# Optimization experiments

Measured on AMD Instinct MI355X. Metric: run time of the kernel, lower is better.

The kernel has to match this reference:

```python
import jax, jax.numpy as jnp
import numpy as np

TEMPERATURE = 0.1
MAX_POS = 6
MAX_NEG = 30
POS_NEG_RATIO = 1.0
NEG_K = max(6, MAX_NEG)  # static top-k width for negatives


def setup_inputs() -> dict:
    key = jax.random.key(0)
    k1, k2 = jax.random.split(key)
    K, D = 8192, 256
    features = jax.random.normal(k1, (K, D), dtype=jnp.float32)
    labels = jax.random.randint(k2, (K,), 0, 64, dtype=jnp.int64)
    return {"features": features, "labels": labels}


def reference(features, labels):
    K = features.shape[0]
    # L2-normalize embeddings (F.normalize, dim=1)
    f = features / jnp.clip(jnp.linalg.norm(features, axis=1, keepdims=True), 1e-12)
    sim = jnp.matmul(f, f.T) / TEMPERATURE                      # [K, K]
    sim = sim - jax.lax.stop_gradient(jnp.max(sim, axis=1, keepdims=True))
    exp_sim = jnp.exp(sim)

    eye = jnp.eye(K, dtype=bool)
    same = labels[:, None] == labels[None, :]
    mask_pos = same & ~eye                                      # same label, off-diagonal
    mask_neg = ~same                                            # 1 - mask_pos - eye

    n_pos = jnp.sum(mask_pos, axis=1).astype(jnp.int32)         # [K]
    n_neg = jnp.sum(mask_neg, axis=1).astype(jnp.int32)         # [K]

    # per-anchor dynamic sample counts (vectorized version of the python loop)
    max_pos_i = jnp.minimum(
        n_pos,
        jnp.maximum(1, jnp.minimum(MAX_POS, (n_neg.astype(jnp.float32) * POS_NEG_RATIO).astype(jnp.int32))),
    )
    max_neg_i = jnp.minimum(n_neg, NEG_K)
    valid_row = (n_pos > 0) & (n_neg > 0)
    max_pos_i = jnp.where(valid_row, max_pos_i, 0)
    max_neg_i = jnp.where(valid_row, max_neg_i, 0)

    rows = jnp.arange(K)[:, None]
    neg_inf = jnp.finfo(sim.dtype).min

    # top-k hard positives by similarity, masked to the first max_pos_i ranks
    pos_scores = jnp.where(mask_pos, sim, neg_inf)
    _, pos_idx = jax.lax.top_k(pos_scores, MAX_POS)             # [K, MAX_POS]
    pos_keep = (jnp.arange(MAX_POS)[None, :] < max_pos_i[:, None]).astype(sim.dtype)
    new_mask_pos = jnp.zeros((K, K), sim.dtype).at[rows, pos_idx].add(pos_keep)

    # random negatives: randperm emulated by top-k of uniform scores over neg slots
    rand = jax.random.uniform(jax.random.key(42), (K, K), dtype=jnp.float32)
    neg_scores = jnp.where(mask_neg, rand, -1.0)
    _, neg_idx = jax.lax.top_k(neg_scores, NEG_K)               # [K, NEG_K]
    neg_keep = (jnp.arange(NEG_K)[None, :] < max_neg_i[:, None]).astype(sim.dtype)
    new_mask_neg = jnp.zeros((K, K), sim.dtype).at[rows, neg_idx].add(neg_keep)

    numerator = jnp.sum(exp_sim * new_mask_pos, axis=1)
    denominator = jnp.sum(exp_sim * (new_mask_pos + new_mask_neg), axis=1)
    loss = -jnp.log(jnp.clip(numerator / denominator, 1e-8))
    return jnp.mean(loss)
```

## Files before the change

kernel.cpp:

```cpp
#include <hip/hip_runtime.h>
#include <hip/hip_fp16.h>
#include <math.h>
#include <stdint.h>


#define NEGK 30
#define MAXP 6
#define MAXBC 320
#define GT 64

typedef _Float16 h2v __attribute__((ext_vector_type(2)));
typedef _Float16 f16x8 __attribute__((ext_vector_type(8)));
typedef float f32x16 __attribute__((ext_vector_type(16)));

__device__ __forceinline__ uint64_t mix64(uint64_t z) {
  z += 0x9E3779B97F4A7C15ULL;
  z = (z ^ (z >> 30)) * 0xBF58476D1CE4E5B9ULL;
  z = (z ^ (z >> 27)) * 0x94D049BB133111EBULL;
  return z ^ (z >> 31);
}

__device__ __forceinline__ float wave_reduce_add(float p) {
#pragma unroll
  for (int o = 32; o; o >>= 1) p += __shfl_down(p, o, 64);
  return p;
}

__device__ __forceinline__ float dot8h(uint4 a, uint4 b, float acc) {
  const h2v* pa = (const h2v*)&a;
  const h2v* pb = (const h2v*)&b;
#if __has_builtin(__builtin_amdgcn_fdot2)
#pragma unroll
  for (int q = 0; q < 4; ++q) acc = __builtin_amdgcn_fdot2(pa[q], pb[q], acc, false);
#else
#pragma unroll
  for (int q = 0; q < 4; ++q)
    acc += (float)pa[q].x * (float)pb[q].x + (float)pa[q].y * (float)pb[q].y;
#endif
  return acc;
}

__global__ __launch_bounds__(256) void k_prep(const float* __restrict__ F,
                                              const int* __restrict__ labels, int K,
                                              __half* __restrict__ Fh,
                                              int* __restrict__ g_start,
                                              int* __restrict__ g_soff,
                                              int* __restrict__ g_bucket,
                                              int4* __restrict__ g_meta) {
  __shared__ int cnt[64], start[65], cur[64], soff_s[64];
  const int tid = threadIdx.x;

  if ((int)blockIdx.x < K / 4) {
    const int row = blockIdx.x * 4 + (tid >> 6);
    const int lane = tid & 63;
    const float4 a = ((const float4*)(F + (size_t)row * 256))[lane];
    float p = a.x * a.x + a.y * a.y + a.z * a.z + a.w * a.w;
    p = wave_reduce_add(p);
    p = __shfl(p, 0, 64);
    const float inv = 1.0f / fmaxf(sqrtf(p), 1e-12f);
    union { __half2 h[2]; uint2 u; } cv;
    cv.h[0] = __float22half2_rn(make_float2(a.x * inv, a.y * inv));
    cv.h[1] = __float22half2_rn(make_float2(a.z * inv, a.w * inv));
    ((uint2*)(Fh + (size_t)row * 256))[lane] = cv.u;
    return;
  }

  if (tid < 64) cnt[tid] = 0;
  __syncthreads();
  for (int t = tid; t < K; t += 256) atomicAdd(&cnt[labels[t] & 63], 1);
  __syncthreads();
  if (tid == 0) {
    int acc = 0, sacc = 0;
    for (int l = 0; l < 64; ++l) {
      start[l] = acc;
      const int B = cnt[l];
      acc += B;
      soff_s[l] = sacc;
      const int Bc = B < MAXBC ? B : MAXBC;
      sacc += Bc * Bc;
    }
    start[64] = acc;
  }
  __syncthreads();
  if (tid < 64) { cur[tid] = start[tid]; g_soff[tid] = soff_s[tid]; }
  if (tid < 65) g_start[tid] = start[tid];
  __syncthreads();
  for (int t = tid; t < K; t += 256) {
    const int l = labels[t] & 63;
    const int p = atomicAdd(&cur[l], 1);
    g_bucket[p] = t;
    g_meta[t] = make_int4(start[l], cnt[l], p - start[l], soff_s[l]);
  }
}

__global__ __launch_bounds__(256, 4) void k_gram(const __half* __restrict__ Fh,
                                                 const int* __restrict__ g_start,
                                                 const int* __restrict__ g_soff,
                                                 const int* __restrict__ g_bucket,
                                                 float* __restrict__ g_sims) {
  const int b  = blockIdx.x;
  const int bs = g_start[b];
  const int B  = g_start[b + 1] - bs;
  const int Bc = B < MAXBC ? B : MAXBC;
  if (Bc <= 0) return;
  const int r0 = blockIdx.y * GT;
  const int c0 = blockIdx.z * GT;
  if (r0 >= Bc || c0 >= Bc) return;

  const int tid = threadIdx.x;
  const int wv = tid >> 6, lane = tid & 63;
  const int wr = (wv >> 1) * 32;
  const int wc = (wv & 1) * 32;
  const int rA = r0 + wr + (lane & 31);
  const int rB = c0 + wc + (lane & 31);
  const int kq = lane >> 5;

  const int gA = g_bucket[bs + (rA < Bc ? rA : Bc - 1)];
  const int gB = g_bucket[bs + (rB < Bc ? rB : Bc - 1)];
  const uint4* pA = (const uint4*)(Fh + (size_t)gA * 256) + kq;
  const uint4* pB = (const uint4*)(Fh + (size_t)gB * 256) + kq;

  f32x16 acc;
#pragma unroll
  for (int q = 0; q < 16; ++q) acc[q] = 0.0f;

#pragma unroll
  for (int it = 0; it < 16; ++it) {
    const f16x8 a  = *(const f16x8*)(pA + 2 * it);
    const f16x8 bf = *(const f16x8*)(pB + 2 * it);
    acc = __builtin_amdgcn_mfma_f32_32x32x16_f16(a, bf, acc, 0, 0, 0);
  }

  float* outb = g_sims + g_soff[b];
  const int ccs = c0 + wc + (lane & 31);
  const bool cok = ccs < Bc;
#pragma unroll
  for (int reg = 0; reg < 16; ++reg) {
    const int row = (reg & 3) + 8 * (reg >> 2) + 4 * (lane >> 5);
    const int rrs = r0 + wr + row;
    if (cok && rrs < Bc)
      outb[(size_t)rrs * Bc + ccs] = (rrs == ccs) ? -3.0e38f : acc[reg] * 10.0f;
  }
}

__global__ __launch_bounds__(256) void k_anchor(
    const __half* __restrict__ Fh, const int* __restrict__ g_bucket,
    const int4* __restrict__ g_meta, const float* __restrict__ g_sims,
    float* __restrict__ g_part, int K) {
  __shared__ uint4 sA[4 * 32];
  const int wv = threadIdx.x >> 6;
  const int lane = threadIdx.x & 63;
  const int i = blockIdx.x * 4 + wv;

  ((uint2*)sA)[wv * 64 + lane] = ((const uint2*)(Fh + (size_t)i * 256))[lane];
  const uint4* sw = sA + wv * 32;

  const int4 mt = g_meta[i];
  const int bs = mt.x, B = mt.y;
  const int Bc = B < MAXBC ? B : MAXBC;
  int loc = mt.z;
  if (loc >= Bc) loc = 0;
  const int n_pos = B - 1;
  const int n_neg = K - B;
  const float* simrow = g_sims + mt.w + (size_t)loc * Bc;

  float v[5];
#pragma unroll
  for (int rr = 0; rr < 5; ++rr) {
    const int t = lane + rr * 64;
    v[rr] = (t < Bc) ? simrow[t] : -3.4e38f;
  }

  int t6 = n_neg < MAXP ? n_neg : MAXP;
  if (t6 < 1) t6 = 1;
  int take = n_pos < t6 ? n_pos : t6;
  if (n_pos <= 0 || n_neg <= 0) take = 0;
  const int target = (take > 0) ? (n_neg < NEGK ? n_neg : NEGK) : 0;

  const int s = lane & 3, g = lane >> 2;
  const int n0 = g, n1 = 16 + g;
  const uint64_t z0 = mix64(((uint64_t)(uint32_t)i << 32) | (uint32_t)n0);
  const uint64_t z1 = mix64(((uint64_t)(uint32_t)i << 32) | (uint32_t)n1);
  const unsigned int r0 = (unsigned int)(((uint64_t)(uint32_t)z0 * (uint64_t)n_neg) >> 32);
  const unsigned int r1 = (unsigned int)(((uint64_t)(uint32_t)z1 * (uint64_t)n_neg) >> 32);
  const int pos0 = (r0 < (unsigned int)bs) ? (int)r0 : (int)r0 + B;
  const int pos1 = (r1 < (unsigned int)bs) ? (int)r1 : (int)r1 + B;
  const bool pv0 = (n0 < target), pv1 = (n1 < target);
  const int j0 = pv0 ? g_bucket[pos0] : 0;
  const int j1 = pv1 ? g_bucket[pos1] : 0;
  const uint4* f0 = (const uint4*)(Fh + (size_t)j0 * 256);
  const uint4* f1 = (const uint4*)(Fh + (size_t)j1 * 256);
  float d0 = 0.0f, d1 = 0.0f;
#pragma unroll
  for (int k = 0; k < 8; ++k) {
    const uint4 aw = sw[k * 4 + s];
    d0 = dot8h(f0[k * 4 + s], aw, d0);
    d1 = dot8h(f1[k * 4 + s], aw, d1);
  }
  d0 += __shfl_xor(d0, 1, 64); d0 += __shfl_xor(d0, 2, 64);
  d1 += __shfl_xor(d1, 1, 64); d1 += __shfl_xor(d1, 2, 64);
  float e = 0.0f;
  if (s == 0) {
    if (pv0) e += expf(d0 * 10.0f);
    if (pv1) e += expf(d1 * 10.0f);
  }
  const float wsum = wave_reduce_add(e);

  float num = 0.0f;
  for (int r = 0; r < take; ++r) {
    float best = v[0];
#pragma unroll
    for (int c = 1; c < 5; ++c) best = fmaxf(best, v[c]);
#pragma unroll
    for (int o = 1; o < 64; o <<= 1) best = fmaxf(best, __shfl_xor(best, o, 64));
    num += expf(best);
#pragma unroll
    for (int c = 0; c < 5; ++c)
      if (v[c] == best) v[c] = -3.4e38f;
  }

  if (lane == 0) {
    float ls = 0.0f;
    if (take > 0) {
      const float denom = num + wsum;
      float ratio = denom > 0.0f ? num / denom : 0.0f;
      ratio = fmaxf(ratio, 1e-8f);
      ls = -logf(ratio);
    }
    g_part[i] = ls;
  }
}

__global__ __launch_bounds__(1024) void k_final(const float* __restrict__ g_part,
                                                float* __restrict__ out, int K) {
  __shared__ float s[16];
  float p = 0.0f;
  for (int t = threadIdx.x; t < K; t += 1024) p += g_part[t];
  p = wave_reduce_add(p);
  if ((threadIdx.x & 63) == 0) s[threadIdx.x >> 6] = p;
  __syncthreads();
  if (threadIdx.x == 0) {
    float tot = 0.0f;
#pragma unroll
    for (int w = 0; w < 16; ++w) tot += s[w];
    out[0] = tot / (float)K;
  }
}

extern "C" void kernel_launch(void* const* d_in, const int* in_sizes, int n_in,
                              void* d_out, int out_size, void* d_ws, size_t ws_size,
                              hipStream_t stream) {
  (void)n_in; (void)out_size; (void)ws_size;
  const float* F = (const float*)d_in[0];
  const int* labels = (const int*)d_in[1];
  const int K = in_sizes[1];
  float* out = (float*)d_out;

  char* ws = (char*)d_ws;
  size_t off = 0;
  int*   g_start  = (int*)(ws + off);   off += 512;
  int*   g_soff   = (int*)(ws + off);   off += 256;
  int*   g_bucket = (int*)(ws + off);   off += (size_t)K * 4;
  float* g_part   = (float*)(ws + off); off += (size_t)K * 4;
  off = (off + 255) & ~(size_t)255;
  int4*  g_meta   = (int4*)(ws + off);  off += (size_t)K * 16;
  __half* Fh      = (__half*)(ws + off); off += (size_t)K * 256 * 2;
  float* g_sims   = (float*)(ws + off);  off += (size_t)MAXBC * K * 4;

  k_prep<<<K / 4 + 1, 256, 0, stream>>>(F, labels, K, Fh, g_start, g_soff,
                                        g_bucket, g_meta);
  {
    dim3 grid(64, (MAXBC + GT - 1) / GT, (MAXBC + GT - 1) / GT);
    k_gram<<<grid, 256, 0, stream>>>(Fh, g_start, g_soff, g_bucket, g_sims);
  }
  k_anchor<<<K / 4, 256, 0, stream>>>(Fh, g_bucket, g_meta, g_sims, g_part, K);
  k_final<<<1, 1024, 0, stream>>>(g_part, out, K);
}
```

Before: 107.3 us.

## Fuse gram and anchor kernels into per-label strip kernel with LDS sims

Merges the per-label MFMA gram kernel and the per-anchor loss kernel into one kernel. Each block computes a 32-row strip of the label-group similarity matrix into shared memory and then evaluates the loss for those anchors, eight per wave. This removes the global sims buffer, the per-row metadata array and one kernel launch. The trade-off is fewer active blocks and a serial loop over anchors inside each wave. It also drops the old clamp that mapped rows beyond MAXBC to row 0, so anchors in groups larger than MAXBC would have no loss written.

```diff
diff --git a/kernel.cpp b/kernel.cpp
--- a/kernel.cpp
+++ b/kernel.cpp
@@ -7,7 +7,7 @@
 #define NEGK 30
 #define MAXP 6
 #define MAXBC 320
-#define GT 64
+#define SR 32
 
 typedef _Float16 h2v __attribute__((ext_vector_type(2)));
 typedef _Float16 f16x8 __attribute__((ext_vector_type(8)));
@@ -44,10 +44,8 @@
                                               const int* __restrict__ labels, int K,
                                               __half* __restrict__ Fh,
                                               int* __restrict__ g_start,
-                                              int* __restrict__ g_soff,
-                                              int* __restrict__ g_bucket,
-                                              int4* __restrict__ g_meta) {
-  __shared__ int cnt[64], start[65], cur[64], soff_s[64];
+                                              int* __restrict__ g_bucket) {
+  __shared__ int cnt[64], start[65], cur[64];
   const int tid = threadIdx.x;
 
   if ((int)blockIdx.x < K / 4) {
@@ -70,164 +68,155 @@
   for (int t = tid; t < K; t += 256) atomicAdd(&cnt[labels[t] & 63], 1);
   __syncthreads();
   if (tid == 0) {
-    int acc = 0, sacc = 0;
-    for (int l = 0; l < 64; ++l) {
-      start[l] = acc;
-      const int B = cnt[l];
-      acc += B;
-      soff_s[l] = sacc;
-      const int Bc = B < MAXBC ? B : MAXBC;
-      sacc += Bc * Bc;
-    }
+    int acc = 0;
+    for (int l = 0; l < 64; ++l) { start[l] = acc; acc += cnt[l]; }
     start[64] = acc;
   }
   __syncthreads();
-  if (tid < 64) { cur[tid] = start[tid]; g_soff[tid] = soff_s[tid]; }
+  if (tid < 64) cur[tid] = start[tid];
   if (tid < 65) g_start[tid] = start[tid];
   __syncthreads();
   for (int t = tid; t < K; t += 256) {
     const int l = labels[t] & 63;
     const int p = atomicAdd(&cur[l], 1);
     g_bucket[p] = t;
-    g_meta[t] = make_int4(start[l], cnt[l], p - start[l], soff_s[l]);
-  }
-}
-
-__global__ __launch_bounds__(256, 4) void k_gram(const __half* __restrict__ Fh,
-                                                 const int* __restrict__ g_start,
-                                                 const int* __restrict__ g_soff,
-                                                 const int* __restrict__ g_bucket,
-                                                 float* __restrict__ g_sims) {
+  }
+}
+
+__global__ __launch_bounds__(256, 2) void k_strip(
+    const __half* __restrict__ Fh, const int* __restrict__ g_start,
+    const int* __restrict__ g_bucket, float* __restrict__ g_part, int K) {
+  __shared__ float sims[SR][MAXBC];
+  __shared__ uint4 sAr[4 * 32];
+
   const int b  = blockIdx.x;
   const int bs = g_start[b];
   const int B  = g_start[b + 1] - bs;
   const int Bc = B < MAXBC ? B : MAXBC;
   if (Bc <= 0) return;
-  const int r0 = blockIdx.y * GT;
-  const int c0 = blockIdx.z * GT;
-  if (r0 >= Bc || c0 >= Bc) return;
+  const int r0 = blockIdx.y * SR;
+  if (r0 >= Bc) return;
 
   const int tid = threadIdx.x;
   const int wv = tid >> 6, lane = tid & 63;
-  const int wr = (wv >> 1) * 32;
-  const int wc = (wv & 1) * 32;
-  const int rA = r0 + wr + (lane & 31);
-  const int rB = c0 + wc + (lane & 31);
   const int kq = lane >> 5;
 
-  const int gA = g_bucket[bs + (rA < Bc ? rA : Bc - 1)];
-  const int gB = g_bucket[bs + (rB < Bc ? rB : Bc - 1)];
-  const uint4* pA = (const uint4*)(Fh + (size_t)gA * 256) + kq;
-  const uint4* pB = (const uint4*)(Fh + (size_t)gB * 256) + kq;
-
-  f32x16 acc;
-#pragma unroll
-  for (int q = 0; q < 16; ++q) acc[q] = 0.0f;
-
-#pragma unroll
-  for (int it = 0; it < 16; ++it) {
-    const f16x8 a  = *(const f16x8*)(pA + 2 * it);
-    const f16x8 bf = *(const f16x8*)(pB + 2 * it);
-    acc = __builtin_amdgcn_mfma_f32_32x32x16_f16(a, bf, acc, 0, 0, 0);
-  }
-
-  float* outb = g_sims + g_soff[b];
-  const int ccs = c0 + wc + (lane & 31);
-  const bool cok = ccs < Bc;
-#pragma unroll
-  for (int reg = 0; reg < 16; ++reg) {
-    const int row = (reg & 3) + 8 * (reg >> 2) + 4 * (lane >> 5);
-    const int rrs = r0 + wr + row;
-    if (cok && rrs < Bc)
-      outb[(size_t)rrs * Bc + ccs] = (rrs == ccs) ? -3.0e38f : acc[reg] * 10.0f;
-  }
-}
-
-__global__ __launch_bounds__(256) void k_anchor(
-    const __half* __restrict__ Fh, const int* __restrict__ g_bucket,
-    const int4* __restrict__ g_meta, const float* __restrict__ g_sims,
-    float* __restrict__ g_part, int K) {
-  __shared__ uint4 sA[4 * 32];
-  const int wv = threadIdx.x >> 6;
-  const int lane = threadIdx.x & 63;
-  const int i = blockIdx.x * 4 + wv;
-
-  ((uint2*)sA)[wv * 64 + lane] = ((const uint2*)(Fh + (size_t)i * 256))[lane];
-  const uint4* sw = sA + wv * 32;
-
-  const int4 mt = g_meta[i];
-  const int bs = mt.x, B = mt.y;
-  const int Bc = B < MAXBC ? B : MAXBC;
-  int loc = mt.z;
-  if (loc >= Bc) loc = 0;
+  {
+    const int rA = r0 + (lane & 31);
+    const int gA = g_bucket[bs + (rA < Bc ? rA : Bc - 1)];
+    const uint4* pA = (const uint4*)(Fh + (size_t)gA * 256) + kq;
+    uint4 afr[16];
+#pragma unroll
+    for (int it = 0; it < 16; ++it) afr[it] = pA[2 * it];
+
+    for (int ct = wv; ct * 32 < Bc; ct += 4) {
+      const int rB = ct * 32 + (lane & 31);
+      const int gB = g_bucket[bs + (rB < Bc ? rB : Bc - 1)];
+      const uint4* pB = (const uint4*)(Fh + (size_t)gB * 256) + kq;
+
+      f32x16 acc;
+#pragma unroll
+      for (int q = 0; q < 16; ++q) acc[q] = 0.0f;
+#pragma unroll
+      for (int it = 0; it < 16; ++it) {
+        const f16x8 a  = *(const f16x8*)&afr[it];
+        const f16x8 bf = *(const f16x8*)(pB + 2 * it);
+        acc = __builtin_amdgcn_mfma_f32_32x32x16_f16(a, bf, acc, 0, 0, 0);
+      }
+
+      const int ccs = ct * 32 + (lane & 31);
+      if (ccs < Bc) {
+#pragma unroll
+        for (int reg = 0; reg < 16; ++reg) {
+          const int row = (reg & 3) + 8 * (reg >> 2) + 4 * (lane >> 5);
+          const int rrs = r0 + row;
+          sims[row][ccs] = (rrs == ccs) ? -3.0e38f : acc[reg] * 10.0f;
+        }
+      }
+    }
+  }
+  __syncthreads();
+
+  const int na = (Bc - r0) < SR ? (Bc - r0) : SR;
   const int n_pos = B - 1;
   const int n_neg = K - B;
-  const float* simrow = g_sims + mt.w + (size_t)loc * Bc;
-
-  float v[5];
-#pragma unroll
-  for (int rr = 0; rr < 5; ++rr) {
-    const int t = lane + rr * 64;
-    v[rr] = (t < Bc) ? simrow[t] : -3.4e38f;
-  }
-
-  int t6 = n_neg < MAXP ? n_neg : MAXP;
-  if (t6 < 1) t6 = 1;
-  int take = n_pos < t6 ? n_pos : t6;
-  if (n_pos <= 0 || n_neg <= 0) take = 0;
-  const int target = (take > 0) ? (n_neg < NEGK ? n_neg : NEGK) : 0;
-
-  const int s = lane & 3, g = lane >> 2;
-  const int n0 = g, n1 = 16 + g;
-  const uint64_t z0 = mix64(((uint64_t)(uint32_t)i << 32) | (uint32_t)n0);
-  const uint64_t z1 = mix64(((uint64_t)(uint32_t)i << 32) | (uint32_t)n1);
-  const unsigned int r0 = (unsigned int)(((uint64_t)(uint32_t)z0 * (uint64_t)n_neg) >> 32);
-  const unsigned int r1 = (unsigned int)(((uint64_t)(uint32_t)z1 * (uint64_t)n_neg) >> 32);
-  const int pos0 = (r0 < (unsigned int)bs) ? (int)r0 : (int)r0 + B;
-  const int pos1 = (r1 < (unsigned int)bs) ? (int)r1 : (int)r1 + B;
-  const bool pv0 = (n0 < target), pv1 = (n1 < target);
-  const int j0 = pv0 ? g_bucket[pos0] : 0;
-  const int j1 = pv1 ? g_bucket[pos1] : 0;
-  const uint4* f0 = (const uint4*)(Fh + (size_t)j0 * 256);
-  const uint4* f1 = (const uint4*)(Fh + (size_t)j1 * 256);
-  float d0 = 0.0f, d1 = 0.0f;
-#pragma unroll
-  for (int k = 0; k < 8; ++k) {
-    const uint4 aw = sw[k * 4 + s];
-    d0 = dot8h(f0[k * 4 + s], aw, d0);
-    d1 = dot8h(f1[k * 4 + s], aw, d1);
-  }
-  d0 += __shfl_xor(d0, 1, 64); d0 += __shfl_xor(d0, 2, 64);
-  d1 += __shfl_xor(d1, 1, 64); d1 += __shfl_xor(d1, 2, 64);
-  float e = 0.0f;
-  if (s == 0) {
-    if (pv0) e += expf(d0 * 10.0f);
-    if (pv1) e += expf(d1 * 10.0f);
-  }
-  const float wsum = wave_reduce_add(e);
-
-  float num = 0.0f;
-  for (int r = 0; r < take; ++r) {
-    float best = v[0];
-#pragma unroll
-    for (int c = 1; c < 5; ++c) best = fmaxf(best, v[c]);
-#pragma unroll
-    for (int o = 1; o < 64; o <<= 1) best = fmaxf(best, __shfl_xor(best, o, 64));
-    num += expf(best);
-#pragma unroll
-    for (int c = 0; c < 5; ++c)
-      if (v[c] == best) v[c] = -3.4e38f;
-  }
-
-  if (lane == 0) {
-    float ls = 0.0f;
-    if (take > 0) {
-      const float denom = num + wsum;
-      float ratio = denom > 0.0f ? num / denom : 0.0f;
-      ratio = fmaxf(ratio, 1e-8f);
-      ls = -logf(ratio);
-    }
-    g_part[i] = ls;
+  uint4* swv = sAr + wv * 32;
+
+  for (int a8 = 0; a8 < 8; ++a8) {
+    const int a = wv * 8 + a8;
+    if (a >= na) break;
+    const int i = g_bucket[bs + r0 + a];
+
+    ((uint2*)swv)[lane] = ((const uint2*)(Fh + (size_t)i * 256))[lane];
+
+    float v[5];
+#pragma unroll
+    for (int rr = 0; rr < 5; ++rr) {
+      const int t = lane + rr * 64;
+      v[rr] = (t < Bc) ? sims[a][t] : -3.4e38f;
+    }
+
+    int t6 = n_neg < MAXP ? n_neg : MAXP;
+    if (t6 < 1) t6 = 1;
+    int take = n_pos < t6 ? n_pos : t6;
+    if (n_pos <= 0 || n_neg <= 0) take = 0;
+    const int target = (take > 0) ? (n_neg < NEGK ? n_neg : NEGK) : 0;
+
+    const int s = lane & 3, g = lane >> 2;
+    const int n0 = g, n1 = 16 + g;
+    const uint64_t z0 = mix64(((uint64_t)(uint32_t)i << 32) | (uint32_t)n0);
+    const uint64_t z1 = mix64(((uint64_t)(uint32_t)i << 32) | (uint32_t)n1);
+    const unsigned int rr0 = (unsigned int)(((uint64_t)(uint32_t)z0 * (uint64_t)n_neg) >> 32);
+    const unsigned int rr1 = (unsigned int)(((uint64_t)(uint32_t)z1 * (uint64_t)n_neg) >> 32);
+    const int pos0 = (rr0 < (unsigned int)bs) ? (int)rr0 : (int)rr0 + B;
+    const int pos1 = (rr1 < (unsigned int)bs) ? (int)rr1 : (int)rr1 + B;
+    const bool pv0 = (n0 < target), pv1 = (n1 < target);
+    const int j0 = pv0 ? g_bucket[pos0] : 0;
+    const int j1 = pv1 ? g_bucket[pos1] : 0;
+    const uint4* f0 = (const uint4*)(Fh + (size_t)j0 * 256);
+    const uint4* f1 = (const uint4*)(Fh + (size_t)j1 * 256);
+    uint4 c0a[8], c1a[8];
+#pragma unroll
+    for (int k = 0; k < 8; ++k) { c0a[k] = f0[k * 4 + s]; c1a[k] = f1[k * 4 + s]; }
+    float d0 = 0.0f, d1 = 0.0f;
+#pragma unroll
+    for (int k = 0; k < 8; ++k) {
+      const uint4 aw = swv[k * 4 + s];
+      d0 = dot8h(c0a[k], aw, d0);
+      d1 = dot8h(c1a[k], aw, d1);
+    }
+    d0 += __shfl_xor(d0, 1, 64); d0 += __shfl_xor(d0, 2, 64);
+    d1 += __shfl_xor(d1, 1, 64); d1 += __shfl_xor(d1, 2, 64);
+    float e = 0.0f;
+    if (s == 0) {
+      if (pv0) e += expf(d0 * 10.0f);
+      if (pv1) e += expf(d1 * 10.0f);
+    }
+    const float wsum = wave_reduce_add(e);
+
+    float num = 0.0f;
+    for (int r = 0; r < take; ++r) {
+      float best = v[0];
+#pragma unroll
+      for (int c = 1; c < 5; ++c) best = fmaxf(best, v[c]);
+#pragma unroll
+      for (int o = 1; o < 64; o <<= 1) best = fmaxf(best, __shfl_xor(best, o, 64));
+      num += expf(best);
+#pragma unroll
+      for (int c = 0; c < 5; ++c)
+        if (v[c] == best) v[c] = -3.4e38f;
+    }
+
+    if (lane == 0) {
+      float ls = 0.0f;
+      if (take > 0) {
+        const float denom = num + wsum;
+        float ratio = denom > 0.0f ? num / denom : 0.0f;
+        ratio = fmaxf(ratio, 1e-8f);
+        ls = -logf(ratio);
+      }
+      g_part[i] = ls;
+    }
   }
 }
 
@@ -259,20 +248,15 @@
   char* ws = (char*)d_ws;
   size_t off = 0;
   int*   g_start  = (int*)(ws + off);   off += 512;
-  int*   g_soff   = (int*)(ws + off);   off += 256;
   int*   g_bucket = (int*)(ws + off);   off += (size_t)K * 4;
   float* g_part   = (float*)(ws + off); off += (size_t)K * 4;
   off = (off + 255) & ~(size_t)255;
-  int4*  g_meta   = (int4*)(ws + off);  off += (size_t)K * 16;
   __half* Fh      = (__half*)(ws + off); off += (size_t)K * 256 * 2;
-  float* g_sims   = (float*)(ws + off);  off += (size_t)MAXBC * K * 4;
-
-  k_prep<<<K / 4 + 1, 256, 0, stream>>>(F, labels, K, Fh, g_start, g_soff,
-                                        g_bucket, g_meta);
+
+  k_prep<<<K / 4 + 1, 256, 0, stream>>>(F, labels, K, Fh, g_start, g_bucket);
   {
-    dim3 grid(64, (MAXBC + GT - 1) / GT, (MAXBC + GT - 1) / GT);
-    k_gram<<<grid, 256, 0, stream>>>(Fh, g_start, g_soff, g_bucket, g_sims);
-  }
-  k_anchor<<<K / 4, 256, 0, stream>>>(Fh, g_bucket, g_meta, g_sims, g_part, K);
+    dim3 grid(64, (MAXBC + SR - 1) / SR);
+    k_strip<<<grid, 256, 0, stream>>>(Fh, g_start, g_bucket, g_part, K);
+  }
   k_final<<<1, 1024, 0, stream>>>(g_part, out, K);
 }
```

Result: slower. 119.6 us (+11.4%).
